# Kernel tuning notes

Hardware: AMD Instinct MI355X
Metric: run time of the kernel (lower is better)

Reference implementation:

```python
import jax, jax.numpy as jnp
import numpy as np

B, N, H, HID, L = 16, 256, 1024, 300, 64


def setup_inputs() -> dict:
    key = jax.random.key(0)
    ks = jax.random.split(key, 10)
    s = 0.02
    inp = {}
    inp["input"] = jax.random.normal(ks[0], (B, N, H), jnp.float32)
    # variable-length valid-token mask (first tokens always valid)
    lengths = jax.random.randint(ks[1], (B,), N // 2, N + 1)
    inp["logits_mask"] = jnp.arange(N)[None, :] < lengths[:, None]
    inp["labels"] = jax.random.randint(ks[2], (B, N, N), 0, L)
    inp["mlp_h_W"] = jax.random.normal(ks[3], (HID, H), jnp.float32) * s
    inp["mlp_h_b"] = jnp.zeros((HID,), jnp.float32)
    inp["mlp_d_W"] = jax.random.normal(ks[4], (HID, H), jnp.float32) * s
    inp["mlp_d_b"] = jnp.zeros((HID,), jnp.float32)
    # Bilinear with bias_x=bias_y=True -> weight [L, HID+1, HID+1]
    inp["bilinear_W"] = jax.random.normal(ks[5], (L, HID + 1, HID + 1), jnp.float32) * s
    inp["start_trans"] = jax.random.normal(ks[6], (L,), jnp.float32) * 0.1
    inp["trans"] = jax.random.normal(ks[7], (L, L), jnp.float32) * 0.1
    inp["end_trans"] = jax.random.normal(ks[8], (L,), jnp.float32) * 0.1
    return inp


def reference(input, logits_mask, labels, mlp_h_W, mlp_h_b, mlp_d_W, mlp_d_b,
              bilinear_W, start_trans, trans, end_trans):
    # --- biaffine scores (dropout is identity in eval) ---
    rel_h = jax.nn.relu(input @ mlp_h_W.T + mlp_h_b)            # [B,N,HID]
    rel_d = jax.nn.relu(input @ mlp_d_W.T + mlp_d_b)            # [B,N,HID]
    ones = jnp.ones((B, N, 1), rel_h.dtype)
    h1 = jnp.concatenate([rel_h, ones], -1)                     # [B,N,HID+1]
    d1 = jnp.concatenate([rel_d, ones], -1)
    # rel_atten(rel_d, rel_h) -> [B,L,Nd,Nh]; permute -> [B,Nd,Nh,L]
    s_rel = jnp.einsum('bxi,lij,byj->bxyl', d1, bilinear_W, h1)  # [B,N,N,L]

    # --- masked flatten: instead of compacting rows (data-dependent shape),
    # keep all B*N rows and weight each row's contribution by index = mask[:,0].
    # Mathematically identical to the torch compaction. ---
    s_flat = s_rel.reshape(B * N, N, L)
    emissions = jax.nn.log_softmax(s_flat, -1)                  # [M,N,L]
    crf_mask = jnp.broadcast_to(logits_mask[:, None, :], (B, N, N)).reshape(B * N, N)
    row_w = logits_mask.reshape(-1).astype(emissions.dtype)     # index = mask[:,0]
    tags = labels.reshape(B * N, N)
    mf = crf_mask.astype(emissions.dtype)

    # --- CRF numerator (vectorized, no recurrence) ---
    emit_sc = jnp.take_along_axis(emissions, tags[..., None], -1)[..., 0]  # [M,N]
    num = start_trans[tags[:, 0]] + (emit_sc * mf).sum(-1)
    num = num + (trans[tags[:, :-1], tags[:, 1:]] * mf[:, 1:]).sum(-1)
    last_idx = crf_mask.sum(-1).astype(jnp.int32) - 1
    last_tags = jnp.take_along_axis(tags, last_idx[:, None], 1)[:, 0]
    num = num + end_trans[last_tags]

    # --- CRF partition function via scan ---
    alpha0 = start_trans[None, :] + emissions[:, 0]             # [M,L]
    e_seq = emissions[:, 1:].swapaxes(0, 1)                     # [N-1,M,L]
    m_seq = crf_mask[:, 1:].swapaxes(0, 1)                      # [N-1,M]

    def fwd_step(alpha, xs):
        e_t, m_t = xs
        nxt = jax.nn.logsumexp(alpha[:, :, None] + trans[None], axis=1) + e_t
        return jnp.where(m_t[:, None], nxt, alpha), None

    alpha, _ = jax.lax.scan(fwd_step, alpha0, (e_seq, m_seq))
    den = jax.nn.logsumexp(alpha + end_trans[None, :], -1)
    loss = -((num - den) * row_w).sum()                         # reduction='sum'

    # --- Viterbi decode (padded; frozen tag repeated past seq end) ---
    ar = jnp.arange(L)

    def vit_step(score, xs):
        e_t, m_t = xs
        sc = score[:, :, None] + trans[None]                    # [M,L_prev,L_cur]
        idx = jnp.argmax(sc, axis=1)                            # [M,L]
        nxt = jnp.max(sc, axis=1) + e_t
        hist = jnp.where(m_t[:, None], idx, ar[None, :])
        return jnp.where(m_t[:, None], nxt, score), hist

    score, hist = jax.lax.scan(vit_step, alpha0, (e_seq, m_seq))
    last = jnp.argmax(score + end_trans[None, :], -1)           # [M]

    def btk(cur, h):
        prev = jnp.take_along_axis(h, cur[:, None], 1)[:, 0]
        return prev, prev

    _, rev = jax.lax.scan(btk, last, hist, reverse=True)        # [N-1,M]
    decoded = jnp.concatenate([rev.swapaxes(0, 1), last[:, None]], axis=1)  # [M,N]
    return loss, s_flat, decoded
```

## Files before the change

kernel.cpp:

```cpp
#include <hip/hip_runtime.h>
#include <math.h>


typedef short bf16x8 __attribute__((ext_vector_type(8)));
typedef float f32x4 __attribute__((ext_vector_type(4)));

__device__ __forceinline__ float rlf(float v, int l) {
    return __uint_as_float(__builtin_amdgcn_readlane(__float_as_uint(v), (unsigned)l));
}
__device__ __forceinline__ int rli(int v, int l) {
    return __builtin_amdgcn_readlane(v, (unsigned)l);
}
__device__ __forceinline__ unsigned short f2bf(float x) {
    union { float f; unsigned u; } c; c.f = x;
    unsigned r = c.u + 0x7FFF + ((c.u >> 16) & 1);
    return (unsigned short)(r >> 16);
}
__device__ __forceinline__ float bf2f(unsigned short h) {
    union { unsigned u; float f; } c; c.u = ((unsigned)h) << 16; return c.f;
}
__device__ __forceinline__ void gload16(const void* g, const void* lds) {
    __builtin_amdgcn_global_load_lds(
        (const __attribute__((address_space(1))) void*)g,
        (__attribute__((address_space(3))) void*)lds, 16, 0, 0);
}

__global__ void mask_cvt_kernel(const void* __restrict__ mraw, int* __restrict__ maskI,
                                int* __restrict__ lenB) {
    int b = blockIdx.x, t = threadIdx.x;
    int i = b * 256 + t;
    unsigned int w0 = ((const unsigned int*)mraw)[0];
    int v;
    if (w0 == 1u)               v = ((const int*)mraw)[i];
    else if (w0 == 0x3F800000u) v = (((const float*)mraw)[i] != 0.f) ? 1 : 0;
    else                        v = ((const unsigned char*)mraw)[i] ? 1 : 0;
    maskI[i] = v;
    __shared__ int sh[4];
    int s = v;
    #pragma unroll
    for (int m = 32; m; m >>= 1) s += __shfl_xor(s, m);
    if ((t & 63) == 0) sh[t >> 6] = s;
    __syncthreads();
    if (t == 0) lenB[b] = sh[0] + sh[1] + sh[2] + sh[3];
}

__global__ __launch_bounds__(256)
void wsplit_kernel(const float* __restrict__ Wbil,
                   unsigned short* __restrict__ Wbh, unsigned short* __restrict__ Wbl) {
    __shared__ float Tile[304][17];
    const int l = blockIdx.x, jt = blockIdx.y, t = threadIdx.x;
    const int j0 = jt * 16;
    {
        int jj = t & 15, it = t >> 4;
        #pragma unroll
        for (int ib = 0; ib < 19; ++ib) {
            int i = ib * 16 + it;
            float v = 0.f;
            if (i < 301 && j0 + jj < 301)
                v = Wbil[(size_t)l * 90601 + (size_t)i * 301 + j0 + jj];
            Tile[i][jj] = v;
        }
    }
    __syncthreads();
    {
        int il = t & 15, jj = t >> 4;
        #pragma unroll
        for (int ib = 0; ib < 19; ++ib) {
            int i = ib * 16 + il;
            float v = Tile[i][jj];
            unsigned short hi = f2bf(v);
            unsigned short lo = f2bf(v - bf2f(hi));
            size_t o = ((size_t)(l * 304 + j0 + jj)) * 304 + i;
            Wbh[o] = hi; Wbl[o] = lo;
        }
    }
}

__global__ __launch_bounds__(256)
void mlp_kernel(const float* __restrict__ A,
                const float* __restrict__ Wh, const float* __restrict__ bh_,
                const float* __restrict__ Wd, const float* __restrict__ bd_,
                unsigned short* __restrict__ h1h, unsigned short* __restrict__ h1l,
                unsigned short* __restrict__ d1h, unsigned short* __restrict__ d1l) {
    constexpr int BM = 128, BN = 128, BK = 16;
    __shared__ float As[BK][BM + 4];
    __shared__ float Bs[BK][BN + 4];

    const int t = threadIdx.x;
    const int tn = t & 15, tm = t >> 4;
    const size_t a_row0 = (size_t)blockIdx.x * BM;
    const int n0 = blockIdx.y * BN;
    const int z = blockIdx.z;
    const float* Bm = z ? Wd : Wh;
    const float* bias = z ? bd_ : bh_;
    unsigned short* Ch = z ? d1h : h1h;
    unsigned short* Cl = z ? d1l : h1l;

    float acc[2][2][4][4] = {};
    const int ar = t >> 2, ak = (t & 3) * 4;

    for (int k0 = 0; k0 < 1024; k0 += BK) {
        {
            const float* ap = A + (a_row0 + ar) * 1024 + k0 + ak;
            float4 v0 = *(const float4*)ap;
            float4 v1 = *(const float4*)(ap + 64 * 1024);
            As[ak + 0][ar] = v0.x; As[ak + 1][ar] = v0.y;
            As[ak + 2][ar] = v0.z; As[ak + 3][ar] = v0.w;
            As[ak + 0][64 + ar] = v1.x; As[ak + 1][64 + ar] = v1.y;
            As[ak + 2][64 + ar] = v1.z; As[ak + 3][64 + ar] = v1.w;
        }
        {
            int r1 = min(n0 + ar, 299), r2 = min(n0 + 64 + ar, 299);
            const float* q1 = Bm + (size_t)r1 * 1024 + k0 + ak;
            const float* q2 = Bm + (size_t)r2 * 1024 + k0 + ak;
            float4 v0 = *(const float4*)q1;
            float4 v1 = *(const float4*)q2;
            Bs[ak + 0][ar] = v0.x; Bs[ak + 1][ar] = v0.y;
            Bs[ak + 2][ar] = v0.z; Bs[ak + 3][ar] = v0.w;
            Bs[ak + 0][64 + ar] = v1.x; Bs[ak + 1][64 + ar] = v1.y;
            Bs[ak + 2][64 + ar] = v1.z; Bs[ak + 3][64 + ar] = v1.w;
        }
        __syncthreads();
        #pragma unroll
        for (int kk = 0; kk < BK; ++kk) {
            float4 a0 = *(const float4*)&As[kk][tm * 4];
            float4 a1 = *(const float4*)&As[kk][64 + tm * 4];
            float4 b0 = *(const float4*)&Bs[kk][tn * 4];
            float4 b1 = *(const float4*)&Bs[kk][64 + tn * 4];
            float av[2][4] = {{a0.x, a0.y, a0.z, a0.w}, {a1.x, a1.y, a1.z, a1.w}};
            float bv[2][4] = {{b0.x, b0.y, b0.z, b0.w}, {b1.x, b1.y, b1.z, b1.w}};
            #pragma unroll
            for (int ih = 0; ih < 2; ++ih)
                #pragma unroll
                for (int ii = 0; ii < 4; ++ii)
                    #pragma unroll
                    for (int jh = 0; jh < 2; ++jh)
                        #pragma unroll
                        for (int jj = 0; jj < 4; ++jj)
                            acc[ih][jh][ii][jj] =
                                fmaf(av[ih][ii], bv[jh][jj], acc[ih][jh][ii][jj]);
        }
        __syncthreads();
    }

    #pragma unroll
    for (int ih = 0; ih < 2; ++ih) {
        #pragma unroll
        for (int ii = 0; ii < 4; ++ii) {
            int r = ih * 64 + tm * 4 + ii;
            #pragma unroll
            for (int jh = 0; jh < 2; ++jh) {
                int n = n0 + jh * 64 + tn * 4;
                if (n < 304) {
                    float o[4];
                    #pragma unroll
                    for (int q = 0; q < 4; ++q) {
                        int nq = n + q;
                        float v = acc[ih][jh][ii][q];
                        o[q] = (nq < 300) ? fmaxf(v + bias[min(nq, 299)], 0.f)
                                          : ((nq == 300) ? 1.f : 0.f);
                    }
                    ushort4 h4, l4;
                    h4.x = f2bf(o[0]); l4.x = f2bf(o[0] - bf2f(h4.x));
                    h4.y = f2bf(o[1]); l4.y = f2bf(o[1] - bf2f(h4.y));
                    h4.z = f2bf(o[2]); l4.z = f2bf(o[2] - bf2f(h4.z));
                    h4.w = f2bf(o[3]); l4.w = f2bf(o[3] - bf2f(h4.w));
                    size_t base = (a_row0 + r) * 304 + n;
                    *(ushort4*)&Ch[base] = h4;
                    *(ushort4*)&Cl[base] = l4;
                }
            }
        }
    }
}

template <int MODE>
__global__ __launch_bounds__(256)
void gemm_mfma(const unsigned short* __restrict__ Ah, const unsigned short* __restrict__ Al,
               const unsigned short* __restrict__ Bh, const unsigned short* __restrict__ Bl,
               float* __restrict__ outF, unsigned short* __restrict__ outUh,
               unsigned short* __restrict__ outUl, int c0) {
    __shared__ short Als[128 * 64];
    __shared__ short Bls[128 * 64];

    const int t = threadIdx.x;
    const int lane = t & 63;
    const int w = t >> 6, wr = w >> 1, wc = w & 1;
    const int bx = blockIdx.x, n0 = blockIdx.y * 128;

    int arow0, brow0;
    if constexpr (MODE == 1) {
        arow0 = c0 * 256 + bx * 128;
        brow0 = n0;
    } else {
        int z = blockIdx.z;
        arow0 = (c0 + z) * 256 + bx * 128;
        brow0 = z * 16384 + n0;
    }

    int kcd[4];
    size_t rowA[4], rowB[4];
    const short* ldsA[4];
    const short* ldsB[4];
    #pragma unroll
    for (int c4 = 0; c4 < 4; ++c4) {
        int ch = c4 * 256 + t;
        int r = ch >> 3;
        kcd[c4] = (ch & 7) ^ (r & 7);
        rowA[c4] = (size_t)(arow0 + r) * 304;
        rowB[c4] = (size_t)(brow0 + r) * 304;
        int wavebase = (c4 * 256 + (t & ~63)) * 8;
        ldsA[c4] = &Als[wavebase];
        ldsB[c4] = &Bls[wavebase];
    }

    f32x4 acc[4][4];
    #pragma unroll
    for (int i = 0; i < 4; ++i)
        #pragma unroll
        for (int j = 0; j < 4; ++j)
            acc[i][j] = (f32x4){0.f, 0.f, 0.f, 0.f};

    const int rowA_l = wr * 64 + (lane & 15);
    const int rowB_l = wc * 64 + (lane & 15);
    const int csub = lane >> 4;
    const int cxor = lane & 7;

    for (int it = 0; it < 19; ++it) {
        const int it8 = it * 8;
        #pragma unroll
        for (int c4 = 0; c4 < 4; ++c4) {
            int kg = it8 + kcd[c4];
            {
                int c76 = kg - ((kg >= 76) ? 76 : 0);
                bool hi = c76 < 38;
                const unsigned short* sa =
                    (hi ? Ah : Al) + rowA[c4] + (size_t)(hi ? c76 : c76 - 38) * 8;
                gload16(sa, ldsA[c4]);
            }
            {
                const unsigned short* sb;
                if (kg < 38)       sb = Bh + rowB[c4] + (size_t)kg * 8;
                else if (kg < 76)  sb = Bh + rowB[c4] + (size_t)(kg - 38) * 8;
                else if (kg < 114) sb = Bl + rowB[c4] + (size_t)(kg - 76) * 8;
                else               sb = Bl + rowB[c4] + (size_t)(kg - 114) * 8;
                gload16(sb, ldsB[c4]);
            }
        }
        __syncthreads();

        #pragma unroll
        for (int kh = 0; kh < 2; ++kh) {
            const int kcr = ((kh * 4 + csub) ^ cxor) * 8;
            bf16x8 af[4], bfr[4];
            #pragma unroll
            for (int f = 0; f < 4; ++f)
                af[f] = *(const bf16x8*)&Als[(rowA_l + f * 16) * 64 + kcr];
            #pragma unroll
            for (int f = 0; f < 4; ++f)
                bfr[f] = *(const bf16x8*)&Bls[(rowB_l + f * 16) * 64 + kcr];
            #pragma unroll
            for (int fr = 0; fr < 4; ++fr)
                #pragma unroll
                for (int fb = 0; fb < 4; ++fb)
                    acc[fr][fb] = __builtin_amdgcn_mfma_f32_16x16x32_bf16(
                        af[fr], bfr[fb], acc[fr][fb], 0, 0, 0);
        }
        __syncthreads();
    }

    const int mbase = bx * 128 + wr * 64 + ((lane >> 4) << 2);
    const int nbase = n0 + wc * 64 + (lane & 15);
    #pragma unroll
    for (int fb = 0; fb < 4; ++fb) {
        const int n = nbase + fb * 16;
        if constexpr (MODE == 1) {
            const int ltag = (int)(((unsigned)(n >> 4) * 27595u) >> 19);
            const int j = n - ltag * 304;
            #pragma unroll
            for (int fr = 0; fr < 4; ++fr) {
                #pragma unroll
                for (int reg = 0; reg < 4; ++reg) {
                    int xloc = mbase + fr * 16 + reg;
                    float v = acc[fr][fb][reg];
                    unsigned short hi = f2bf(v);
                    unsigned short lo = f2bf(v - bf2f(hi));
                    size_t o = ((size_t)xloc * 64 + ltag) * 304 + j;
                    outUh[o] = hi;
                    outUl[o] = lo;
                }
            }
        } else {
            const int xx = n >> 6, lt = n & 63;
            const size_t sbase = (size_t)(c0 + blockIdx.z) * 4194304 +
                                 (size_t)xx * 16384 + lt;
            #pragma unroll
            for (int fr = 0; fr < 4; ++fr) {
                #pragma unroll
                for (int reg = 0; reg < 4; ++reg) {
                    int y = mbase + fr * 16 + reg;
                    outF[sbase + (size_t)y * 64] = acc[fr][fb][reg];
                }
            }
        }
    }
}

__global__ __launch_bounds__(256, 3)
void fwd_kernel(const float* __restrict__ s_flat, const int* __restrict__ lenB,
                const int* __restrict__ maskI, const int* __restrict__ labels,
                const float* __restrict__ trans, const float* __restrict__ start_trans,
                const float* __restrict__ end_trans, float* __restrict__ rowterm) {
    __shared__ float T[4096];
    const int t = threadIdx.x;
    for (int i = t; i < 4096; i += 256) T[i] = trans[i];
    __syncthreads();

    const int lane = t & 63, wid = t >> 6;
    const int row = blockIdx.x * 4 + wid;
    if (maskI[row] == 0) {
        if (lane == 0) rowterm[row] = 0.f;
        return;
    }
    const int b = row >> 8;
    const int len = lenB[b];
    const float* srow = s_flat + (size_t)row * 16384;
    const int* lrow = labels + (size_t)row * 256;

    float Ec[64];
    #pragma unroll
    for (int p = 0; p < 64; ++p) Ec[p] = __expf(T[p * 64 + lane]);

    const float et = end_trans[lane];

    float sv = srow[lane];
    int tagprev = lrow[0];
    float num = start_trans[tagprev] + rlf(sv, tagprev);
    float alpha = start_trans[lane] + sv;

    float sv_pre = srow[64 + lane];

    for (int y = 1; y < len; ++y) {
        sv = sv_pre;
        int ynext = (y + 1 < len) ? (y + 1) : (len - 1);
        sv_pre = srow[ynext * 64 + lane];

        const int tag = lrow[y];
        num += rlf(sv, tag) + T[tagprev * 64 + tag];
        tagprev = tag;

        float am = alpha;
        #pragma unroll
        for (int m = 32; m; m >>= 1) am = fmaxf(am, __shfl_xor(am, m));
        float ea = __expf(alpha - am);
        float a0 = 0.f, a1 = 0.f, a2 = 0.f, a3 = 0.f;
        #pragma unroll
        for (int p = 0; p < 64; p += 4) {
            a0 = fmaf(rlf(ea, p + 0), Ec[p + 0], a0);
            a1 = fmaf(rlf(ea, p + 1), Ec[p + 1], a1);
            a2 = fmaf(rlf(ea, p + 2), Ec[p + 2], a2);
            a3 = fmaf(rlf(ea, p + 3), Ec[p + 3], a3);
        }
        alpha = am + __logf((a0 + a1) + (a2 + a3)) + sv;
    }

    num += end_trans[tagprev];

    float da = alpha + et;
    float dmx = da;
    #pragma unroll
    for (int m = 32; m; m >>= 1) dmx = fmaxf(dmx, __shfl_xor(dmx, m));
    float ds = __expf(da - dmx);
    #pragma unroll
    for (int m = 32; m; m >>= 1) ds += __shfl_xor(ds, m);
    float den = dmx + __logf(ds);

    if (lane == 0) rowterm[row] = num - den;
}

__global__ __launch_bounds__(256, 3)
void vitf_kernel(const float* __restrict__ s_flat, const int* __restrict__ lenB,
                 const float* __restrict__ trans, const float* __restrict__ start_trans,
                 const float* __restrict__ end_trans, float* __restrict__ vsb,
                 float* __restrict__ decoded) {
    const int t = threadIdx.x;
    const int lane = t & 63, wid = t >> 6;
    const int row = blockIdx.x * 4 + wid;
    const int len = lenB[row >> 8];
    const float* srow = s_flat + (size_t)row * 16384;
    float* vrow = vsb + (size_t)row * 16384;

    float sv = srow[lane];
    float vs = start_trans[lane] + sv;
    float sv_pre = srow[64 + lane];

    for (int y = 1; y < len; ++y) {
        vrow[(y - 1) * 64 + lane] = vs;
        float svc = sv_pre;
        int ynext = (y + 1 < len) ? (y + 1) : (len - 1);
        sv_pre = srow[ynext * 64 + lane];

        float m0 = -3.4e38f, m1 = -3.4e38f, m2 = -3.4e38f, m3 = -3.4e38f;
        #pragma unroll
        for (int p = 0; p < 64; p += 8) {
            float t0 = rlf(vs, p + 0) + trans[(p + 0) * 64 + lane];
            float t1 = rlf(vs, p + 1) + trans[(p + 1) * 64 + lane];
            m0 = fmaxf(fmaxf(t0, t1), m0);
            float t2 = rlf(vs, p + 2) + trans[(p + 2) * 64 + lane];
            float t3 = rlf(vs, p + 3) + trans[(p + 3) * 64 + lane];
            m1 = fmaxf(fmaxf(t2, t3), m1);
            float t4 = rlf(vs, p + 4) + trans[(p + 4) * 64 + lane];
            float t5 = rlf(vs, p + 5) + trans[(p + 5) * 64 + lane];
            m2 = fmaxf(fmaxf(t4, t5), m2);
            float t6 = rlf(vs, p + 6) + trans[(p + 6) * 64 + lane];
            float t7 = rlf(vs, p + 7) + trans[(p + 7) * 64 + lane];
            m3 = fmaxf(fmaxf(t6, t7), m3);
        }
        vs = fmaxf(fmaxf(m0, m1), fmaxf(m2, m3)) + svc;
    }

    float fe = vs + end_trans[lane];
    float mx = fe;
    #pragma unroll
    for (int m = 32; m; m >>= 1) mx = fmaxf(mx, __shfl_xor(mx, m));
    unsigned long long msk = __ballot(fe == mx);
    int fi = (int)__builtin_ctzll(msk);

    if (lane == 0) decoded[(size_t)row * 256 + 255] = (float)fi;
}

__global__ __launch_bounds__(256)
void vitb_kernel(const float* __restrict__ vsb, const int* __restrict__ lenB,
                 const float* __restrict__ trans, float* __restrict__ decoded) {
    __shared__ float Tt[64][65];
    const int t = threadIdx.x;
    for (int i = t; i < 4096; i += 256) {
        int p = i >> 6, c = i & 63;
        Tt[c][p] = trans[i];
    }
    __syncthreads();

    const int lane = t & 63, wid = t >> 6;
    const int row = blockIdx.x * 4 + wid;
    const int len = lenB[row >> 8];
    const float* vrow = vsb + (size_t)row * 16384;
    float* drow = decoded + (size_t)row * 256;

    int cur = (int)drow[255];

    for (int y = len - 1 + lane; y < 255; y += 64) drow[y] = (float)cur;

    float v0 = vrow[(len - 2) * 64 + lane];
    float v1 = (len >= 3) ? vrow[(len - 3) * 64 + lane] : 0.f;

    for (int y = len - 2; y >= 0; --y) {
        float vy = v0;
        v0 = v1;
        v1 = (y >= 2) ? vrow[(y - 2) * 64 + lane] : 0.f;

        float tp = vy + Tt[cur][lane];
        float mx = tp;
        #pragma unroll
        for (int m = 32; m; m >>= 1) mx = fmaxf(mx, __shfl_xor(mx, m));
        unsigned long long msk = __ballot(tp == mx);
        cur = (int)__builtin_ctzll(msk);
        if (lane == 0) drow[y] = (float)cur;
    }
}

__global__ __launch_bounds__(256, 3)
void vit_kernel(const float* __restrict__ s_flat, const int* __restrict__ lenB,
                const float* __restrict__ trans, const float* __restrict__ start_trans,
                const float* __restrict__ end_trans, unsigned char* __restrict__ hist,
                float* __restrict__ decoded) {
    const int t = threadIdx.x;
    const int lane = t & 63, wid = t >> 6;
    const int row = blockIdx.x * 4 + wid;
    const int len = lenB[row >> 8];
    const float* srow = s_flat + (size_t)row * 16384;
    unsigned char* hrow = hist + (size_t)row * 16320;

    float sv = srow[lane];
    float vs = start_trans[lane] + sv;
    float sv_pre = srow[64 + lane];

    for (int y = 1; y < len; ++y) {
        sv = sv_pre;
        int ynext = (y + 1 < len) ? (y + 1) : (len - 1);
        sv_pre = srow[ynext * 64 + lane];

        float b0 = -3.4e38f, b1 = -3.4e38f, b2 = -3.4e38f, b3 = -3.4e38f;
        int i0 = 0, i1 = 1, i2 = 2, i3 = 3;
        #pragma unroll
        for (int p = 0; p < 64; p += 4) {
            float t0 = rlf(vs, p + 0) + trans[(p + 0) * 64 + lane]; if (t0 > b0) { b0 = t0; i0 = p + 0; }
            float t1 = rlf(vs, p + 1) + trans[(p + 1) * 64 + lane]; if (t1 > b1) { b1 = t1; i1 = p + 1; }
            float t2 = rlf(vs, p + 2) + trans[(p + 2) * 64 + lane]; if (t2 > b2) { b2 = t2; i2 = p + 2; }
            float t3 = rlf(vs, p + 3) + trans[(p + 3) * 64 + lane]; if (t3 > b3) { b3 = t3; i3 = p + 3; }
        }
        bool c;
        c = (b1 > b0) || (b1 == b0 && i1 < i0);
        float bA = c ? b1 : b0; int iA = c ? i1 : i0;
        c = (b3 > b2) || (b3 == b2 && i3 < i2);
        float bB = c ? b3 : b2; int iB = c ? i3 : i2;
        c = (bB > bA) || (bB == bA && iB < iA);
        float bbv = c ? bB : bA; int bi = c ? iB : iA;

        hrow[(size_t)(y - 1) * 64 + lane] = (unsigned char)bi;
        vs = bbv + sv;
    }

    float fv = vs + end_trans[lane]; int fi = lane;
    #pragma unroll
    for (int m = 32; m; m >>= 1) {
        float ov = __shfl_xor(fv, m);
        int oi = __shfl_xor(fi, m);
        bool cc = (ov > fv) || (ov == fv && oi < fi);
        fv = cc ? ov : fv; fi = cc ? oi : fi;
    }

    if (lane == 0) decoded[(size_t)row * 256 + 255] = (float)fi;
}

__global__ __launch_bounds__(256)
void backtrack_kernel(const unsigned char* __restrict__ hist, const int* __restrict__ lenB,
                      float* __restrict__ decoded) {
    const int lane = threadIdx.x & 63, wid = threadIdx.x >> 6;
    const int row = blockIdx.x * 4 + wid;
    const int len = lenB[row >> 8];
    const unsigned char* hrow = hist + (size_t)row * 16320;
    float* drow = decoded + (size_t)row * 256;

    int cur = (int)drow[255];
    for (int y = len - 1 + lane; y < 255; y += 64) drow[y] = (float)cur;

    int t0 = len - 2;
    int c0 = (int)hrow[(t0 - 0) * 64 + lane];
    int c1 = (int)hrow[(t0 - 1) * 64 + lane];
    int c2 = (int)hrow[(t0 - 2) * 64 + lane];
    int c3 = (int)hrow[(t0 - 3) * 64 + lane];

    for (int y = t0; y >= 0; y -= 4) {
        int yn = y - 4;
        int n0 = 0, n1 = 0, n2 = 0, n3 = 0;
        if (yn - 0 >= 0) n0 = (int)hrow[(yn - 0) * 64 + lane];
        if (yn - 1 >= 0) n1 = (int)hrow[(yn - 1) * 64 + lane];
        if (yn - 2 >= 0) n2 = (int)hrow[(yn - 2) * 64 + lane];
        if (yn - 3 >= 0) n3 = (int)hrow[(yn - 3) * 64 + lane];

        cur = rli(c0, cur);
        if (lane == 0) drow[y] = (float)cur;
        if (y - 1 >= 0) { cur = rli(c1, cur); if (lane == 0) drow[y - 1] = (float)cur; }
        if (y - 2 >= 0) { cur = rli(c2, cur); if (lane == 0) drow[y - 2] = (float)cur; }
        if (y - 3 >= 0) { cur = rli(c3, cur); if (lane == 0) drow[y - 3] = (float)cur; }

        c0 = n0; c1 = n1; c2 = n2; c3 = n3;
    }
}

__global__ void loss_kernel(const float* __restrict__ rowterm, float* __restrict__ out) {
    __shared__ float wsum[4];
    int t = threadIdx.x;
    float s = 0.f;
    for (int i = t; i < 4096; i += 256) s += rowterm[i];
    #pragma unroll
    for (int m = 32; m; m >>= 1) s += __shfl_xor(s, m);
    if ((t & 63) == 0) wsum[t >> 6] = s;
    __syncthreads();
    if (t == 0) out[0] = -(wsum[0] + wsum[1] + wsum[2] + wsum[3]);
}

extern "C" void kernel_launch(void* const* d_in, const int* in_sizes, int n_in,
                              void* d_out, int out_size, void* d_ws, size_t ws_size,
                              hipStream_t stream) {
    const float* input  = (const float*)d_in[0];
    const void*  mraw   = d_in[1];
    const int*   labels = (const int*)d_in[2];
    const float* Wh_in  = (const float*)d_in[3];
    const float* bh     = (const float*)d_in[4];
    const float* Wd_in  = (const float*)d_in[5];
    const float* bd     = (const float*)d_in[6];
    const float* Wbil   = (const float*)d_in[7];
    const float* stt    = (const float*)d_in[8];
    const float* trans  = (const float*)d_in[9];
    const float* ett    = (const float*)d_in[10];

    float* out     = (float*)d_out;
    float* s_flat  = out + 1;
    float* decoded = out + 1 + (size_t)67108864;

    char* ws = (char*)d_ws;
    size_t off = 0;
    unsigned short* h1h = (unsigned short*)(ws + off); off += (size_t)4096 * 304 * 2;
    unsigned short* h1l = (unsigned short*)(ws + off); off += (size_t)4096 * 304 * 2;
    unsigned short* d1h = (unsigned short*)(ws + off); off += (size_t)4096 * 304 * 2;
    unsigned short* d1l = (unsigned short*)(ws + off); off += (size_t)4096 * 304 * 2;
    unsigned short* Wbh = (unsigned short*)(ws + off); off += (size_t)19456 * 304 * 2;
    unsigned short* Wbl = (unsigned short*)(ws + off); off += (size_t)19456 * 304 * 2;
    int* maskI = (int*)(ws + off); off += 16384;
    int* lenB  = (int*)(ws + off); off += 256;
    float* rowterm = (float*)(ws + off); off += 16384;

    const size_t vsb_bytes = (size_t)4096 * 16384 * 4;
    const size_t hist_bytes = (size_t)4096 * 16320;
    const size_t perb = (size_t)16384 * 304 * 4;

    bool newpath = (ws_size >= off + vsb_bytes + perb);
    float* vsb = nullptr;
    unsigned char* hist = nullptr;
    if (newpath) { vsb  = (float*)(ws + off); off += vsb_bytes; }
    else         { hist = (unsigned char*)(ws + off); off += hist_bytes; }

    unsigned short* Uh = (unsigned short*)(ws + off);
    size_t avail = (ws_size > off) ? ws_size - off : 0;
    int CB = (int)(avail / perb);
    if (CB < 1) CB = 1;
    if (CB > 16) CB = 16;
    unsigned short* Ul = Uh + (size_t)CB * 16384 * 304;

    mask_cvt_kernel<<<16, 256, 0, stream>>>(mraw, maskI, lenB);
    wsplit_kernel<<<dim3(64, 19), 256, 0, stream>>>(Wbil, Wbh, Wbl);
    mlp_kernel<<<dim3(32, 3, 2), 256, 0, stream>>>(input, Wh_in, bh, Wd_in, bd,
                                                   h1h, h1l, d1h, d1l);

    for (int c0 = 0; c0 < 16; c0 += CB) {
        int cb = (CB < 16 - c0) ? CB : (16 - c0);
        gemm_mfma<1><<<dim3(cb * 2, 152), 256, 0, stream>>>(
            d1h, d1l, Wbh, Wbl, nullptr, Uh, Ul, c0);
        gemm_mfma<2><<<dim3(2, 128, cb), 256, 0, stream>>>(
            h1h, h1l, Uh, Ul, s_flat, nullptr, nullptr, c0);
    }

    fwd_kernel<<<1024, 256, 0, stream>>>(s_flat, lenB, maskI, labels, trans, stt, ett,
                                         rowterm);
    if (newpath) {
        vitf_kernel<<<1024, 256, 0, stream>>>(s_flat, lenB, trans, stt, ett, vsb, decoded);
        vitb_kernel<<<1024, 256, 0, stream>>>(vsb, lenB, trans, decoded);
    } else {
        vit_kernel<<<1024, 256, 0, stream>>>(s_flat, lenB, trans, stt, ett, hist, decoded);
        backtrack_kernel<<<1024, 256, 0, stream>>>(hist, lenB, decoded);
    }
    loss_kernel<<<1, 256, 0, stream>>>(rowterm, out);
}
```

Before: 1.454 ms.

## Drop lo*lo term in split-bf16 GEMMs and flatten intermediate U layout

The split-precision GEMMs previously accumulated all four hi/lo cross products (K=4*304). They now compute only hi*hi, lo*hi and hi*lo, padding the remaining chunks with a zero buffer, which cuts K iterations from 19 to 15. The intermediate U tensor is stored as a flat [x, L*304] row instead of a per-tag padded layout, so address math is simpler and the second GEMM indexes it directly. Viterbi and forward kernels also get a higher occupancy hint in launch_bounds. Dropping the lo*lo term adds a small numerical error, and the tighter register budget may cause spills.

```diff
diff --git a/kernel.cpp b/kernel.cpp
--- a/kernel.cpp
+++ b/kernel.cpp
@@ -26,8 +26,9 @@
 }
 
 __global__ void mask_cvt_kernel(const void* __restrict__ mraw, int* __restrict__ maskI,
-                                int* __restrict__ lenB) {
+                                int* __restrict__ lenB, int* __restrict__ zbuf) {
     int b = blockIdx.x, t = threadIdx.x;
+    if (b == 0 && t < 8) zbuf[t] = 0;
     int i = b * 256 + t;
     unsigned int w0 = ((const unsigned int*)mraw)[0];
     int v;
@@ -179,7 +180,8 @@
 void gemm_mfma(const unsigned short* __restrict__ Ah, const unsigned short* __restrict__ Al,
                const unsigned short* __restrict__ Bh, const unsigned short* __restrict__ Bl,
                float* __restrict__ outF, unsigned short* __restrict__ outUh,
-               unsigned short* __restrict__ outUl, int c0) {
+               unsigned short* __restrict__ outUl, const unsigned short* __restrict__ zbuf,
+               int c0) {
     __shared__ short Als[128 * 64];
     __shared__ short Bls[128 * 64];
 
@@ -188,14 +190,11 @@
     const int w = t >> 6, wr = w >> 1, wc = w & 1;
     const int bx = blockIdx.x, n0 = blockIdx.y * 128;
 
-    int arow0, brow0;
+    int arow0;
     if constexpr (MODE == 1) {
         arow0 = c0 * 256 + bx * 128;
-        brow0 = n0;
     } else {
-        int z = blockIdx.z;
-        arow0 = (c0 + z) * 256 + bx * 128;
-        brow0 = z * 16384 + n0;
+        arow0 = (c0 + blockIdx.z) * 256 + bx * 128;
     }
 
     int kcd[4];
@@ -208,7 +207,13 @@
         int r = ch >> 3;
         kcd[c4] = (ch & 7) ^ (r & 7);
         rowA[c4] = (size_t)(arow0 + r) * 304;
-        rowB[c4] = (size_t)(brow0 + r) * 304;
+        if constexpr (MODE == 1) {
+            rowB[c4] = (size_t)(n0 + r) * 304;
+        } else {
+            int rb = n0 + r;
+            rowB[c4] = (size_t)(blockIdx.z * 256 + (rb >> 6)) * 19456 +
+                       (size_t)(rb & 63) * 304;
+        }
         int wavebase = (c4 * 256 + (t & ~63)) * 8;
         ldsA[c4] = &Als[wavebase];
         ldsB[c4] = &Bls[wavebase];
@@ -226,16 +231,17 @@
     const int csub = lane >> 4;
     const int cxor = lane & 7;
 
-    for (int it = 0; it < 19; ++it) {
+    for (int it = 0; it < 15; ++it) {
         const int it8 = it * 8;
         #pragma unroll
         for (int c4 = 0; c4 < 4; ++c4) {
             int kg = it8 + kcd[c4];
             {
-                int c76 = kg - ((kg >= 76) ? 76 : 0);
-                bool hi = c76 < 38;
-                const unsigned short* sa =
-                    (hi ? Ah : Al) + rowA[c4] + (size_t)(hi ? c76 : c76 - 38) * 8;
+                const unsigned short* sa;
+                if (kg < 38)       sa = Ah + rowA[c4] + (size_t)kg * 8;
+                else if (kg < 76)  sa = Al + rowA[c4] + (size_t)(kg - 38) * 8;
+                else if (kg < 114) sa = Ah + rowA[c4] + (size_t)(kg - 76) * 8;
+                else               sa = zbuf;
                 gload16(sa, ldsA[c4]);
             }
             {
@@ -243,7 +249,7 @@
                 if (kg < 38)       sb = Bh + rowB[c4] + (size_t)kg * 8;
                 else if (kg < 76)  sb = Bh + rowB[c4] + (size_t)(kg - 38) * 8;
                 else if (kg < 114) sb = Bl + rowB[c4] + (size_t)(kg - 76) * 8;
-                else               sb = Bl + rowB[c4] + (size_t)(kg - 114) * 8;
+                else               sb = zbuf;
                 gload16(sb, ldsB[c4]);
             }
         }
@@ -275,8 +281,6 @@
     for (int fb = 0; fb < 4; ++fb) {
         const int n = nbase + fb * 16;
         if constexpr (MODE == 1) {
-            const int ltag = (int)(((unsigned)(n >> 4) * 27595u) >> 19);
-            const int j = n - ltag * 304;
             #pragma unroll
             for (int fr = 0; fr < 4; ++fr) {
                 #pragma unroll
@@ -285,7 +289,7 @@
                     float v = acc[fr][fb][reg];
                     unsigned short hi = f2bf(v);
                     unsigned short lo = f2bf(v - bf2f(hi));
-                    size_t o = ((size_t)xloc * 64 + ltag) * 304 + j;
+                    size_t o = (size_t)xloc * 19456 + n;
                     outUh[o] = hi;
                     outUl[o] = lo;
                 }
@@ -306,7 +310,7 @@
     }
 }
 
-__global__ __launch_bounds__(256, 3)
+__global__ __launch_bounds__(256, 4)
 void fwd_kernel(const float* __restrict__ s_flat, const int* __restrict__ lenB,
                 const int* __restrict__ maskI, const int* __restrict__ labels,
                 const float* __restrict__ trans, const float* __restrict__ start_trans,
@@ -378,7 +382,7 @@
     if (lane == 0) rowterm[row] = num - den;
 }
 
-__global__ __launch_bounds__(256, 3)
+__global__ __launch_bounds__(256, 4)
 void vitf_kernel(const float* __restrict__ s_flat, const int* __restrict__ lenB,
                  const float* __restrict__ trans, const float* __restrict__ start_trans,
                  const float* __restrict__ end_trans, float* __restrict__ vsb,
@@ -599,11 +603,12 @@
     unsigned short* Wbl = (unsigned short*)(ws + off); off += (size_t)19456 * 304 * 2;
     int* maskI = (int*)(ws + off); off += 16384;
     int* lenB  = (int*)(ws + off); off += 256;
+    int* zbuf  = (int*)(ws + off); off += 256;
     float* rowterm = (float*)(ws + off); off += 16384;
 
     const size_t vsb_bytes = (size_t)4096 * 16384 * 4;
     const size_t hist_bytes = (size_t)4096 * 16320;
-    const size_t perb = (size_t)16384 * 304 * 4;
+    const size_t perb = (size_t)256 * 19456 * 2 * 2;
 
     bool newpath = (ws_size >= off + vsb_bytes + perb);
     float* vsb = nullptr;
@@ -616,9 +621,9 @@
     int CB = (int)(avail / perb);
     if (CB < 1) CB = 1;
     if (CB > 16) CB = 16;
-    unsigned short* Ul = Uh + (size_t)CB * 16384 * 304;
-
-    mask_cvt_kernel<<<16, 256, 0, stream>>>(mraw, maskI, lenB);
+    unsigned short* Ul = Uh + (size_t)CB * 256 * 19456;
+
+    mask_cvt_kernel<<<16, 256, 0, stream>>>(mraw, maskI, lenB, zbuf);
     wsplit_kernel<<<dim3(64, 19), 256, 0, stream>>>(Wbil, Wbh, Wbl);
     mlp_kernel<<<dim3(32, 3, 2), 256, 0, stream>>>(input, Wh_in, bh, Wd_in, bd,
                                                    h1h, h1l, d1h, d1l);
@@ -626,9 +631,9 @@
     for (int c0 = 0; c0 < 16; c0 += CB) {
         int cb = (CB < 16 - c0) ? CB : (16 - c0);
         gemm_mfma<1><<<dim3(cb * 2, 152), 256, 0, stream>>>(
-            d1h, d1l, Wbh, Wbl, nullptr, Uh, Ul, c0);
+            d1h, d1l, Wbh, Wbl, nullptr, Uh, Ul, (const unsigned short*)zbuf, c0);
         gemm_mfma<2><<<dim3(2, 128, cb), 256, 0, stream>>>(
-            h1h, h1l, Uh, Ul, s_flat, nullptr, nullptr, c0);
+            h1h, h1l, Uh, Ul, s_flat, nullptr, nullptr, (const unsigned short*)zbuf, c0);
     }
 
     fwd_kernel<<<1024, 256, 0, stream>>>(s_flat, lenB, maskI, labels, trans, stt, ett,
```

Result: faster. 1.334 ms (-8.3%).
